# Kernel optimization log

Measured on AMD Instinct MI355X. Metric: run time of the kernel, lower is better.

The kernel has to match this reference:

```python
import jax, jax.numpy as jnp
import numpy as np

H, L, N = 512, 4096, 64

def make_dplr_hippo(n):
    # HiPPO-LegS -> NPLR -> DPLR diagonalization (numpy, init-time only)
    p0 = np.sqrt(1 + 2 * np.arange(n))
    A = p0[:, None] * p0[None, :]
    A = -(np.tril(A) - np.diag(np.arange(n)))
    p = np.sqrt(np.arange(n) + 0.5)
    b = np.sqrt(2 * np.arange(n) + 1.0)
    S = A + p[:, None] * p[None, :]
    Lambda_re = np.full(n, np.diagonal(S).mean())
    Lambda_im, V = np.linalg.eigh(S * -1j)
    Pc = V.conj().T @ p
    Bc = V.conj().T @ b
    return Lambda_re, Lambda_im, Pc, Bc

def setup_inputs() -> dict:
    key = jax.random.key(0)
    k_u, k_c, k_s = jax.random.split(key, 3)
    lr, li, Pc, Bc = make_dplr_hippo(N)
    tile = lambda v: jnp.tile(jnp.asarray(v, jnp.float32)[None, :], (H, 1))
    dt_min, dt_max = 0.001, 0.1
    log_step = (jax.random.uniform(k_s, (H, 1), jnp.float32)
                * (np.log(dt_max) - np.log(dt_min)) + np.log(dt_min))
    return {
        "u": jax.random.normal(k_u, (H, L), jnp.float32),
        "Lambda_re": tile(lr), "Lambda_im": tile(li),
        "P_re": tile(Pc.real), "P_im": tile(Pc.imag),
        "B_re": tile(Bc.real), "B_im": tile(Bc.imag),
        "C": jax.random.normal(k_c, (H, N, 2), jnp.float32) * (0.5 ** 0.5),
        "D": jnp.ones((H, 1), jnp.float32),
        "log_step": log_step,
    }

def reference(u, Lambda_re, Lambda_im, P_re, P_im, B_re, B_im, C, D, log_step):
    # u: [H, L]; all params leading dim H (vmapped channels)
    Lam = jnp.minimum(Lambda_re, -1e-4) + 1j * Lambda_im      # [H, N]
    P = P_re + 1j * P_im                                       # [H, N]
    B = B_re + 1j * B_im                                       # [H, N]
    Cc = C[..., 0] + 1j * C[..., 1]                             # [H, N]
    step = jnp.exp(log_step)                                    # [H, 1]
    Lseq = u.shape[-1]
    Omega = jnp.exp(-2j * jnp.pi * (jnp.arange(Lseq) / Lseq)).astype(jnp.complex64)  # [L]
    g = (2.0 / step) * ((1.0 - Omega) / (1.0 + Omega))[None, :]  # [H, L]
    c = 2.0 / (1.0 + Omega)                                      # [L]
    denom = 1.0 / (g[:, :, None] - Lam[:, None, :])              # [H, L, N]
    cauchy = lambda v: jnp.einsum('hn,hln->hl', v, denom)
    k00 = cauchy(Cc.conj() * B)
    k01 = cauchy(Cc.conj() * P)
    k10 = cauchy(P.conj() * B)
    k11 = cauchy(P.conj() * P)
    atRoots = c[None, :] * (k00 - k01 * (1.0 / (1.0 + k11)) * k10)
    K = jnp.fft.ifft(atRoots, Lseq, axis=-1).real                # [H, L] conv kernel
    # causal convolution via zero-padded FFT (length 2L)
    ud = jnp.fft.rfft(u, n=2 * Lseq, axis=-1)
    Kd = jnp.fft.rfft(K, n=2 * Lseq, axis=-1)
    y = jnp.fft.irfft(ud * Kd, n=2 * Lseq, axis=-1)[..., :Lseq]
    return y + D * u
```

## Files before the change

### kernel.cpp

```cpp
#include <hip/hip_runtime.h>
#include <math.h>

#define NT 512

typedef float v2 __attribute__((ext_vector_type(2)));

__device__ __forceinline__ v2 vrot(v2 a){ return (v2){-a.y, a.x}; }
__device__ __forceinline__ v2 vconj(v2 a){ return (v2){a.x, -a.y}; }

__device__ __forceinline__ v2 pk_addrot(v2 a, v2 b){
    v2 d;
    asm("v_pk_add_f32 %0, %1, %2 op_sel:[0,1] op_sel_hi:[1,0] neg_lo:[0,1] neg_hi:[0,0]"
        : "=v"(d) : "v"(a), "v"(b));
    return d;
}
__device__ __forceinline__ v2 pk_subrot(v2 a, v2 b){
    v2 d;
    asm("v_pk_add_f32 %0, %1, %2 op_sel:[0,1] op_sel_hi:[1,0] neg_lo:[0,0] neg_hi:[0,1]"
        : "=v"(d) : "v"(a), "v"(b));
    return d;
}
__device__ __forceinline__ v2 vcmul(v2 a, v2 b){
    v2 d;
    asm("v_pk_mul_f32 %0, %1, %2 op_sel:[0,0] op_sel_hi:[0,1]"
        : "=v"(d) : "v"(a), "v"(b));
    asm("v_pk_fma_f32 %0, %1, %2, %0 op_sel:[1,1,0] op_sel_hi:[1,0,1] neg_lo:[0,1,0] neg_hi:[0,0,0]"
        : "+v"(d) : "v"(a), "v"(b));
    return d;
}
__device__ __forceinline__ v2 vcmulc(v2 a, v2 b){
    v2 d;
    asm("v_pk_mul_f32 %0, %1, %2 op_sel:[0,0] op_sel_hi:[0,1] neg_lo:[0,0] neg_hi:[0,1]"
        : "=v"(d) : "v"(a), "v"(b));
    asm("v_pk_fma_f32 %0, %1, %2, %0 op_sel:[1,1,0] op_sel_hi:[1,0,1]"
        : "+v"(d) : "v"(a), "v"(b));
    return d;
}

__device__ __forceinline__ v2 pk_add_bh(v2 a, v2 s){
    v2 d;
    asm("v_pk_add_f32 %0, %1, %2 op_sel:[0,1] op_sel_hi:[1,1]"
        : "=v"(d) : "v"(a), "s"(s));
    return d;
}
__device__ __forceinline__ v2 pk_fma_sq_bh(v2 a, v2 s){
    v2 d;
    asm("v_pk_fma_f32 %0, %1, %1, %2 op_sel:[0,0,1] op_sel_hi:[1,1,1]"
        : "=v"(d) : "v"(a), "s"(s));
    return d;
}
__device__ __forceinline__ v2 pk_mul_cross(v2 a){
    v2 d;
    asm("v_pk_mul_f32 %0, %1, %1 op_sel:[1,0] op_sel_hi:[0,1]"
        : "=v"(d) : "v"(a));
    return d;
}
__device__ __forceinline__ v2 pk_inv_lo(v2 rr, v2 dd){
    v2 d;
    asm("v_pk_mul_f32 %0, %1, %2 op_sel:[0,1] op_sel_hi:[0,0]"
        : "=v"(d) : "v"(rr), "v"(dd));
    return d;
}
__device__ __forceinline__ v2 pk_inv_hi(v2 rr, v2 dd){
    v2 d;
    asm("v_pk_mul_f32 %0, %1, %2 op_sel:[1,1] op_sel_hi:[1,0]"
        : "=v"(d) : "v"(rr), "v"(dd));
    return d;
}
__device__ __forceinline__ v2 pk_mul_bl(v2 a, v2 s){
    v2 d;
    asm("v_pk_mul_f32 %0, %1, %2 op_sel:[0,0] op_sel_hi:[1,0]"
        : "=v"(d) : "v"(a), "s"(s));
    return d;
}
__device__ __forceinline__ v2 pk_mulp(v2 a, v2 b){
    v2 d;
    asm("v_pk_mul_f32 %0, %1, %2 op_sel:[0,0] op_sel_hi:[1,1]"
        : "=v"(d) : "v"(a), "v"(b));
    return d;
}
__device__ __forceinline__ void fmaBlo(v2& acc, v2 w, v2 p){
    asm("v_pk_fma_f32 %0, %1, %2, %0 op_sel:[0,0,0] op_sel_hi:[0,1,1]"
        : "+v"(acc) : "s"(w), "v"(p));
}
__device__ __forceinline__ void fmaBhi(v2& acc, v2 w, v2 p){
    asm("v_pk_fma_f32 %0, %1, %2, %0 op_sel:[1,0,0] op_sel_hi:[1,1,1]"
        : "+v"(acc) : "s"(w), "v"(p));
}
__device__ __forceinline__ void fmaBlon(v2& acc, v2 w, v2 p){
    asm("v_pk_fma_f32 %0, %1, %2, %0 op_sel:[0,0,0] op_sel_hi:[0,1,1] neg_lo:[1,0,0] neg_hi:[1,0,0]"
        : "+v"(acc) : "s"(w), "v"(p));
}

__device__ __forceinline__ int SW(int e){ return e ^ (((e>>5) ^ (e>>9)) & 15); }

__device__ __forceinline__ v2& q512(v2* buf, int tbs, int k){
    return *(v2*)((char*)buf + ((tbs ^ (k<<3)) + (k<<12)));
}
__device__ __forceinline__ v2& q512u(v2* buf, int tbs, int k){
    return *(v2*)((char*)buf + (((tbs ^ 64) ^ (k<<3)) + (k<<12) + 32768));
}

__device__ __forceinline__ int d8r4(int x){
    return ((x&7)<<9) | (((x>>3)&7)<<6) | (((x>>6)&7)<<3) | ((x>>9)&7);
}
__device__ __forceinline__ int rev3(int t){
    return ((t&7)<<6) | (t&56) | ((t>>6)&7);
}

__device__ __forceinline__ void load_row(const v2* twd, int rowIdx, v2 W[7]) {
    const float4* rp4 = (const float4*)(twd + rowIdx*8);
    float4 q0 = rp4[0], q1 = rp4[1], q2 = rp4[2], q3 = rp4[3];
    W[0]=(v2){q0.x,q0.y}; W[1]=(v2){q0.z,q0.w}; W[2]=(v2){q1.x,q1.y};
    W[3]=(v2){q1.z,q1.w}; W[4]=(v2){q2.x,q2.y}; W[5]=(v2){q2.z,q2.w};
    W[6]=(v2){q3.x,q3.y};
}

__device__ __forceinline__ void dft8_inv(v2 t[8], v2 y[8]) {
    const float RH = 0.70710678f;
    v2 p  = t[0]+t[4], m  = t[0]-t[4], q  = t[2]+t[6], r  = t[2]-t[6];
    v2 E0 = p+q, E2 = p-q;
    v2 E1 = pk_addrot(m, r), E3 = pk_subrot(m, r);
    v2 p2 = t[1]+t[5], m2 = t[1]-t[5], q2 = t[3]+t[7], r2 = t[3]-t[7];
    v2 O0 = p2+q2, O2 = p2-q2;
    v2 O1 = pk_addrot(m2, r2), O3 = pk_subrot(m2, r2);
    v2 W1O = RH * pk_addrot(O1, O1);
    v2 A3  = RH * pk_addrot(O3, O3);
    y[0] = E0 + O0;  y[4] = E0 - O0;
    y[1] = E1 + W1O; y[5] = E1 - W1O;
    y[2] = pk_addrot(E2, O2); y[6] = pk_subrot(E2, O2);
    y[3] = pk_addrot(E3, A3); y[7] = pk_subrot(E3, A3);
}

__device__ __forceinline__ void dft8_inv_lo4(v2 t[8], v2 y[4]) {
    const float RH = 0.70710678f;
    v2 p  = t[0]+t[4], m  = t[0]-t[4], q  = t[2]+t[6], r  = t[2]-t[6];
    v2 E0 = p+q, E2 = p-q;
    v2 E1 = pk_addrot(m, r), E3 = pk_subrot(m, r);
    v2 p2 = t[1]+t[5], m2 = t[1]-t[5], q2 = t[3]+t[7], r2 = t[3]-t[7];
    v2 O0 = p2+q2, O2 = p2-q2;
    v2 O1 = pk_addrot(m2, r2), O3 = pk_subrot(m2, r2);
    v2 W1O = RH * pk_addrot(O1, O1);
    v2 A3  = RH * pk_addrot(O3, O3);
    y[0] = E0 + O0;
    y[1] = E1 + W1O;
    y[2] = pk_addrot(E2, O2);
    y[3] = pk_addrot(E3, A3);
}

__device__ __forceinline__ void dft8_fwd(v2 t[8], v2 y[8]) {
    const float RH = 0.70710678f;
    v2 p  = t[0]+t[4], m  = t[0]-t[4], q  = t[2]+t[6], r  = t[2]-t[6];
    v2 E0 = p+q, E2 = p-q;
    v2 E1 = pk_subrot(m, r), E3 = pk_addrot(m, r);
    v2 p2 = t[1]+t[5], m2 = t[1]-t[5], q2 = t[3]+t[7], r2 = t[3]-t[7];
    v2 O0 = p2+q2, O2 = p2-q2;
    v2 O1 = pk_subrot(m2, r2), O3 = pk_addrot(m2, r2);
    v2 W1O = RH * pk_subrot(O1, O1);
    v2 A3f = RH * pk_addrot(O3, O3);
    y[0] = E0 + O0;  y[4] = E0 - O0;
    y[1] = E1 + W1O; y[5] = E1 - W1O;
    y[2] = pk_subrot(E2, O2); y[6] = pk_addrot(E2, O2);
    y[3] = E3 - A3f; y[7] = E3 + A3f;
}


template<int Q, bool BAR>
__device__ __forceinline__ void r8_dit_inv(v2* buf, int tid, const v2* twd) {
    int j = tid & (Q-1);
    v2 W[7];
    load_row(twd, (512/Q)*j, W);
    int base = 8*tid - 7*j;
    v2 t[8];
    #pragma unroll
    for (int k = 0; k < 8; ++k) t[k] = buf[SW(base + k*Q)];
    #pragma unroll
    for (int k = 0; k < 7; ++k) t[k+1] = vcmul(t[k+1], W[k]);
    v2 y[8];
    dft8_inv(t, y);
    #pragma unroll
    for (int m = 0; m < 8; ++m) buf[SW(base + m*Q)] = y[m];
    if (BAR) __syncthreads();
    else     __builtin_amdgcn_wave_barrier();
}

template<int Q, bool BAR>
__device__ __forceinline__ void r8_dif_fwd(v2* buf, int tid, const v2* twd) {
    if (Q == 1) {
        const int b0  = tid << 6;
        const int bt  = tid << 3;
        const int mLs = (((bt>>5) ^ (bt>>9)) & 15) << 3;
        const int msU = (mLs ^ 64) + 32768;
        #pragma unroll 1
        for (int hh = 0; hh < 2; ++hh) {
            const int ms = hh ? msU : mLs;
            v2 t[8];
            #pragma unroll
            for (int k = 0; k < 8; ++k)
                t[k] = *(v2*)((char*)buf + ((b0 + (k<<3)) ^ ms));
            v2 y[8];
            dft8_fwd(t, y);
            #pragma unroll
            for (int m = 0; m < 8; ++m)
                *(v2*)((char*)buf + ((b0 + (m<<3)) ^ ms)) = y[m];
        }
        if (BAR) __syncthreads();
        else     __builtin_amdgcn_wave_barrier();
        return;
    }
    int j = tid & (Q-1);
    int baseL = 8*tid - 7*j;
    v2 W[7];
    load_row(twd, (512/Q)*j, W);
    #pragma unroll 1
    for (int hh = 0; hh < 2; ++hh) {
        int base = baseL + (hh << 12);
        v2 t[8];
        #pragma unroll
        for (int k = 0; k < 8; ++k) t[k] = buf[SW(base + k*Q)];
        v2 y[8];
        dft8_fwd(t, y);
        #pragma unroll
        for (int k = 0; k < 7; ++k) y[k+1] = vcmulc(y[k+1], W[k]);
        #pragma unroll
        for (int m = 0; m < 8; ++m) buf[SW(base + m*Q)] = y[m];
    }
    if (BAR) __syncthreads();
    else     __builtin_amdgcn_wave_barrier();
}

__global__ void __launch_bounds__(64)
s4_prep(const float* __restrict__ Lre, const float* __restrict__ Lim,
        const float* __restrict__ Pre, const float* __restrict__ Pim,
        const float* __restrict__ Bre, const float* __restrict__ Bim,
        const float* __restrict__ Cin,
        float* __restrict__ ws8, float* __restrict__ ws1,
        v2* __restrict__ twd)
{
    int b = blockIdx.x;
    if (b == (int)gridDim.x - 1) {
        const float fm = 6.2831853072f / 4096.0f;
        #pragma unroll
        for (int r = 0; r < 8; ++r) {
            int j = r*64 + (int)threadIdx.x;
            #pragma unroll
            for (int k = 0; k < 7; ++k) {
                float s, c; __sincosf(fm * (float)(j*(k+1)), &s, &c);
                twd[j*8 + k] = (v2){c, s};
            }
            twd[j*8 + 7] = (v2){1.0f, 0.0f};
        }
        return;
    }
    int idx = b*64 + threadIdx.x;
    float lre = fminf(Lre[idx], -1e-4f);
    float lim = Lim[idx];
    float pr = Pre[idx], pi = Pim[idx];
    float br = Bre[idx], bi = Bim[idx];
    float cr = Cin[2*idx], ci = Cin[2*idx+1];
    v2 cc = (v2){cr, -ci};
    v2 w00 = vcmul(cc, (v2){br, bi});
    v2 w01 = vcmul(cc, (v2){pr, pi});
    v2 w10 = vcmul((v2){pr,-pi}, (v2){br, bi});
    float* o = ws8 + idx*8;
    o[0] = -lre;  o[1] = -lim;
    o[2] = w00.x; o[3] = w00.y;
    o[4] = w01.x; o[5] = w01.y;
    o[6] = w10.x; o[7] = w10.y;
    ws1[2*idx]   = pr*pr + pi*pi;
    ws1[2*idx+1] = lre*lre;
}

__global__ __attribute__((amdgpu_waves_per_eu(4, 4))) void __launch_bounds__(NT)
s4_fused(const float* __restrict__ u,
         const float* __restrict__ Din, const float* __restrict__ logstep,
         const float* __restrict__ ws8, const float* __restrict__ ws1,
         const v2* __restrict__ twd,
         float* __restrict__ out)
{
    __shared__ v2 buf[8192];
    const int tid = threadIdx.x;
    const int h = blockIdx.x;
    const int tbs = (tid ^ ((tid>>5) & 15)) << 3;

    const float step = expf(logstep[h]);
    const float tos  = 2.0f / step;
    const float hstep = 0.5f * step;
    const float* pp = ws8 + (h*64)*8;
    const float4* pp4 = (const float4*)pp;
    const v2* pw2 = (const v2*)(ws1 + h*128);

    v2 a4[4];
    #pragma unroll 1
    for (int hp = 0; hp < 2; ++hp) {
        v2 tvA, tvB;
        {
            float tv[4];
            #pragma unroll
            for (int i = 0; i < 4; ++i) {
                int l = hp*(4*NT) + i*NT + tid;
                float ang = -6.2831855f * ((float)l * (1.0f/4096.0f));
                float sh, ch; __sincosf(0.5f*ang, &sh, &ch);
                float traw = -tos * sh * __builtin_amdgcn_rcpf(ch);
                tv[i] = fminf(fmaxf(traw, -1e12f), 1e12f);
            }
            tvA = (v2){tv[0], tv[1]};
            tvB = (v2){tv[2], tv[3]};
        }
        v2 aX00A=(v2)(0.f), aY00A=(v2)(0.f), aX00B=(v2)(0.f), aY00B=(v2)(0.f);
        v2 aX01A=(v2)(0.f), aY01A=(v2)(0.f), aX01B=(v2)(0.f), aY01B=(v2)(0.f);
        v2 aX10A=(v2)(0.f), aY10A=(v2)(0.f), aX10B=(v2)(0.f), aY10B=(v2)(0.f);
        v2 aX11A=(v2)(0.f), aY11A=(v2)(0.f), aX11B=(v2)(0.f), aY11B=(v2)(0.f);
        #pragma unroll 2
        for (int n = 0; n < 64; ++n) {
            float4 A = pp4[2*n], Bq = pp4[2*n+1];
            v2 lam = (v2){A.x, A.y};
            v2 w00 = (v2){A.z, A.w};
            v2 w01 = (v2){Bq.x, Bq.y};
            v2 w10 = (v2){Bq.z, Bq.w};
            v2 Wv  = pw2[n];
            v2 sA = pk_add_bh(tvA, lam), sB = pk_add_bh(tvB, lam);
            v2 dA = pk_fma_sq_bh(sA, Wv), dB = pk_fma_sq_bh(sB, Wv);
            v2 PA = pk_mul_cross(dA), PB = pk_mul_cross(dB);
            v2 RR;
            RR.x = __builtin_amdgcn_rcpf(PA.x);
            RR.y = __builtin_amdgcn_rcpf(PB.x);
            v2 invA = pk_inv_lo(RR, dA), invB = pk_inv_hi(RR, dB);
            v2 pxA = pk_mul_bl(invA, lam), pxB = pk_mul_bl(invB, lam);
            v2 pyA = pk_mulp(invA, sA),    pyB = pk_mulp(invB, sB);
            fmaBlo(aX00A, w00, pxA); fmaBhi(aX00A, w00, pyA);
            fmaBhi(aY00A, w00, pxA); fmaBlon(aY00A, w00, pyA);
            fmaBlo(aX00B, w00, pxB); fmaBhi(aX00B, w00, pyB);
            fmaBhi(aY00B, w00, pxB); fmaBlon(aY00B, w00, pyB);
            fmaBlo(aX01A, w01, pxA); fmaBhi(aX01A, w01, pyA);
            fmaBhi(aY01A, w01, pxA); fmaBlon(aY01A, w01, pyA);
            fmaBlo(aX01B, w01, pxB); fmaBhi(aX01B, w01, pyB);
            fmaBhi(aY01B, w01, pxB); fmaBlon(aY01B, w01, pyB);
            fmaBlo(aX10A, w10, pxA); fmaBhi(aX10A, w10, pyA);
            fmaBhi(aY10A, w10, pxA); fmaBlon(aY10A, w10, pyA);
            fmaBlo(aX10B, w10, pxB); fmaBhi(aX10B, w10, pyB);
            fmaBhi(aY10B, w10, pxB); fmaBlon(aY10B, w10, pyB);
            fmaBlo(aX11A, Wv, pxA);  fmaBlon(aY11A, Wv, pyA);
            fmaBlo(aX11B, Wv, pxB);  fmaBlon(aY11B, Wv, pyB);
        }
        float tvv[4] = { tvA.x, tvA.y, tvB.x, tvB.y };
        v2 k00[4] = { {aX00A.x,aY00A.x}, {aX00A.y,aY00A.y},
                      {aX00B.x,aY00B.x}, {aX00B.y,aY00B.y} };
        v2 k01[4] = { {aX01A.x,aY01A.x}, {aX01A.y,aY01A.y},
                      {aX01B.x,aY01B.x}, {aX01B.y,aY01B.y} };
        v2 k10[4] = { {aX10A.x,aY10A.x}, {aX10A.y,aY10A.y},
                      {aX10B.x,aY10B.x}, {aX10B.y,aY10B.y} };
        v2 k11[4] = { {aX11A.x,aY11A.x}, {aX11A.y,aY11A.y},
                      {aX11B.x,aY11B.x}, {aX11B.y,aY11B.y} };
        #pragma unroll
        for (int i = 0; i < 4; ++i) {
            v2 opk = (v2){1.0f + k11[i].x, k11[i].y};
            float iv = __builtin_amdgcn_rcpf(opk.x*opk.x + opk.y*opk.y);
            v2 r11 = vconj(opk) * iv;
            v2 t  = vcmul(vcmul(k01[i], r11), k10[i]);
            v2 cf = (v2){1.0f, tvv[i]*hstep};
            v2 res = vcmul(cf, k00[i] - t);
            if (hp == 0) q512(buf, tbs, i) = res;
            else         a4[i] = res;
        }
    }
    {
        v2 t[8];
        #pragma unroll
        for (int k = 0; k < 4; ++k) t[k] = q512(buf, tbs, k);
        #pragma unroll
        for (int k = 0; k < 4; ++k) t[4+k] = a4[k];
        __syncthreads();
        v2 y[8];
        dft8_inv(t, y);
        const int tb8 = 8*rev3(tid);
        const int b8  = tb8 << 3;
        const int m8s = (((tb8>>5) ^ (tb8>>9)) & 15) << 3;
        #pragma unroll
        for (int m = 0; m < 8; ++m)
            *(v2*)((char*)buf + ((b8 + (m<<3)) ^ m8s)) = y[m];
    }
    __syncthreads();

    r8_dit_inv<8,  false>(buf, tid, twd);
    r8_dit_inv<64, true >(buf, tid, twd);

    {
        v2 W[7];
        load_row(twd, tid, W);
        v2 t[8];
        #pragma unroll
        for (int k = 0; k < 8; ++k) t[k] = q512(buf, tbs, k);
        #pragma unroll
        for (int k = 0; k < 7; ++k) t[k+1] = vcmul(t[k+1], W[k]);
        v2 y[8];
        dft8_inv(t, y);
        float uval[8];
        const float* up = u + h*4096;
        #pragma unroll
        for (int m = 0; m < 8; ++m) uval[m] = up[tid + 512*m];
        float s2, c2; __sincosf(-6.2831853072f/8192.0f*(float)tid, &s2, &c2);
        v2 cur0 = (v2){c2, s2};
        const v2 C16n = (v2){0.92387953f, -0.38268343f};
        v2 zL[8], zU[8];
        {
            v2 cur = cur0;
            #pragma unroll
            for (int k = 0; k < 8; ++k) {
                zL[k] = (v2){uval[k], y[k].x * (1.0f/4096.0f)};
                zU[k] = vcmul(zL[k], cur);
                cur = vcmul(cur, C16n);
            }
        }
        v2 s[8];
        dft8_fwd(zL, s);
        #pragma unroll
        for (int m = 1; m < 8; ++m) s[m] = vcmulc(s[m], W[m-1]);
        #pragma unroll
        for (int m = 0; m < 8; ++m) q512(buf, tbs, m) = s[m];
        dft8_fwd(zU, s);
        #pragma unroll
        for (int m = 1; m < 8; ++m) s[m] = vcmulc(s[m], W[m-1]);
        #pragma unroll
        for (int m = 0; m < 8; ++m) q512u(buf, tbs, m) = s[m];
    }
    __syncthreads();

    r8_dif_fwd<64, false>(buf, tid, twd);
    r8_dif_fwd<8,  false>(buf, tid, twd);
    r8_dif_fwd<1,  true >(buf, tid, twd);

    {
        float sb, cb; __sincosf(6.2831853072f/8192.0f*(float)tid, &sb, &cb);
        v2 cur = (v2){cb, sb};
        const v2 C16p = (v2){0.92387953f, 0.38268343f};
        v2 v[8];
        #pragma unroll 1
        for (int i = 0; i < 8; ++i) {
            int r  = i*NT + tid;
            int par = (r&1)<<12;
            int e1 = par + d8r4(r>>1);
            int e3 = e1 + 4;
            int k2c = 4096 - r;
            int e4 = ((k2c&1)<<12) + d8r4((k2c>>1)&4095);
            int e2 = (r == 0) ? 0 : (e4 + 4);
            v2 za = buf[SW(e1)];
            v2 zb = buf[SW(e2)];
            v2 zc = buf[SW(e3)];
            v2 zd = buf[SW(e4)];
            v2 U1 = 0.5f*(za + vconj(zb));
            v2 K1 = -0.5f*vrot(za - vconj(zb));
            v2 Yr = vcmul(U1, K1);
            v2 U2 = 0.5f*(zc + vconj(zd));
            v2 K2 = -0.5f*vrot(zc - vconj(zd));
            v2 Ys = vcmul(U2, K2);
            v[i] = pk_addrot(Yr + Ys, vcmul(cur, Yr - Ys));
            cur = vcmul(cur, C16p);
        }
        __syncthreads();
        v2 y[8];
        dft8_inv(v, y);
        const int tb8 = 8*rev3(tid);
        const int b8  = tb8 << 3;
        const int m8s = (((tb8>>5) ^ (tb8>>9)) & 15) << 3;
        #pragma unroll
        for (int m = 0; m < 8; ++m)
            *(v2*)((char*)buf + ((b8 + (m<<3)) ^ m8s)) = y[m];
    }
    __syncthreads();

    r8_dit_inv<8,  false>(buf, tid, twd);
    r8_dit_inv<64, true >(buf, tid, twd);

    {
        v2 W[7];
        load_row(twd, tid, W);
        v2 t[8];
        #pragma unroll
        for (int k = 0; k < 8; ++k) t[k] = q512(buf, tbs, k);
        #pragma unroll
        for (int k = 0; k < 7; ++k) t[k+1] = vcmul(t[k+1], W[k]);
        v2 y[4];
        dft8_inv_lo4(t, y);
        const float Dh = Din[h];
        const float sc = 1.0f / 8192.0f;
        const v2* u2 = (const v2*)(u + h*4096);
        v2*     out2 = (v2*)(out + h*4096);
        #pragma unroll
        for (int m = 0; m < 4; ++m) {
            int n = tid + 512*m;
            out2[n] = sc*y[m] + Dh*u2[n];
        }
    }
}

extern "C" void kernel_launch(void* const* d_in, const int* in_sizes, int n_in,
                              void* d_out, int out_size, void* d_ws, size_t ws_size,
                              hipStream_t stream)
{
    const float* u       = (const float*)d_in[0];
    const float* Lre     = (const float*)d_in[1];
    const float* Lim     = (const float*)d_in[2];
    const float* Pre     = (const float*)d_in[3];
    const float* Pim     = (const float*)d_in[4];
    const float* Bre     = (const float*)d_in[5];
    const float* Bim     = (const float*)d_in[6];
    const float* Cin     = (const float*)d_in[7];
    const float* Din     = (const float*)d_in[8];
    const float* logstep = (const float*)d_in[9];
    float* out = (float*)d_out;
    const int H = in_sizes[8];

    float* ws8 = (float*)d_ws;
    float* ws1 = ws8 + (size_t)H*64*8;
    v2*    twd = (v2*)(ws1 + (size_t)H*128);

    hipLaunchKernelGGL(s4_prep, dim3(H + 1), dim3(64), 0, stream,
                       Lre, Lim, Pre, Pim, Bre, Bim, Cin, ws8, ws1, twd);
    hipLaunchKernelGGL(s4_fused, dim3(H), dim3(NT), 0, stream,
                       u, Din, logstep, ws8, ws1, twd, out);
}
```

Measured before the change: 144.3 us.

## Split fused S4 kernel into separate Cauchy and FFT kernels

```diff
diff --git a/kernel.cpp b/kernel.cpp
--- a/kernel.cpp
+++ b/kernel.cpp
@@ -1,7 +1,8 @@
 #include <hip/hip_runtime.h>
 #include <math.h>
 
-#define NT 512
+#define NT  512
+#define NTC 256
 
 typedef float v2 __attribute__((ext_vector_type(2)));
 
@@ -93,14 +94,12 @@
 }
 
 __device__ __forceinline__ int SW(int e){ return e ^ (((e>>5) ^ (e>>9)) & 15); }
-
 __device__ __forceinline__ v2& q512(v2* buf, int tbs, int k){
     return *(v2*)((char*)buf + ((tbs ^ (k<<3)) + (k<<12)));
 }
 __device__ __forceinline__ v2& q512u(v2* buf, int tbs, int k){
     return *(v2*)((char*)buf + (((tbs ^ 64) ^ (k<<3)) + (k<<12) + 32768));
 }
-
 __device__ __forceinline__ int d8r4(int x){
     return ((x&7)<<9) | (((x>>3)&7)<<6) | (((x>>6)&7)<<3) | ((x>>9)&7);
 }
@@ -163,7 +162,6 @@
     y[2] = pk_subrot(E2, O2); y[6] = pk_addrot(E2, O2);
     y[3] = E3 - A3f; y[7] = E3 + A3f;
 }
-
 
 template<int Q, bool BAR>
 __device__ __forceinline__ void r8_dit_inv(v2* buf, int tid, const v2* twd) {
@@ -235,10 +233,12 @@
         const float* __restrict__ Bre, const float* __restrict__ Bim,
         const float* __restrict__ Cin,
         float* __restrict__ ws8, float* __restrict__ ws1,
-        v2* __restrict__ twd)
+        v2* __restrict__ twd, float* __restrict__ tanv,
+        v2* __restrict__ w8192, int full)
 {
     int b = blockIdx.x;
-    if (b == (int)gridDim.x - 1) {
+    int nb = (int)gridDim.x;
+    if (b == nb - 3) {
         const float fm = 6.2831853072f / 4096.0f;
         #pragma unroll
         for (int r = 0; r < 8; ++r) {
@@ -249,6 +249,28 @@
                 twd[j*8 + k] = (v2){c, s};
             }
             twd[j*8 + 7] = (v2){1.0f, 0.0f};
+        }
+        return;
+    }
+    if (b == nb - 2) {
+        if (!full) return;
+        #pragma unroll 1
+        for (int r = 0; r < 64; ++r) {
+            int l = r*64 + (int)threadIdx.x;
+            float ang = -6.2831855f * ((float)l * (1.0f/4096.0f));
+            float sh, ch; __sincosf(0.5f*ang, &sh, &ch);
+            tanv[l] = -sh * __builtin_amdgcn_rcpf(ch);
+        }
+        return;
+    }
+    if (b == nb - 1) {
+        if (!full) return;
+        const float fm2 = 6.2831853072f / 8192.0f;
+        #pragma unroll
+        for (int r = 0; r < 8; ++r) {
+            int j = r*64 + (int)threadIdx.x;
+            float s, c; __sincosf(fm2 * (float)j, &s, &c);
+            w8192[j] = (v2){c, s};
         }
         return;
     }
@@ -269,6 +291,226 @@
     o[6] = w10.x; o[7] = w10.y;
     ws1[2*idx]   = pr*pr + pi*pi;
     ws1[2*idx+1] = lre*lre;
+}
+
+__global__ __attribute__((amdgpu_waves_per_eu(8, 8))) void __launch_bounds__(NTC)
+s4_cauchy(const float* __restrict__ logstep,
+          const float* __restrict__ ws8, const float* __restrict__ ws1,
+          const float* __restrict__ tanv, v2* __restrict__ atR)
+{
+    const int tid = threadIdx.x;
+    const int h   = blockIdx.x;
+    const int qi  = blockIdx.y;
+    const int lbase = qi*1024;
+
+    const float step = expf(logstep[h]);
+    const float tos  = 2.0f / step;
+    const float hstep = 0.5f * step;
+    const float4* pp4 = (const float4*)(ws8 + (h*64)*8);
+    const v2* pw2 = (const v2*)(ws1 + h*128);
+
+    v2 tvA, tvB;
+    {
+        float tv[4];
+        #pragma unroll
+        for (int i = 0; i < 4; ++i) {
+            float tr = tos * tanv[lbase + (i<<8) + tid];
+            tv[i] = fminf(fmaxf(tr, -1e12f), 1e12f);
+        }
+        tvA = (v2){tv[0], tv[1]};
+        tvB = (v2){tv[2], tv[3]};
+    }
+    v2 aX00A=(v2)(0.f), aY00A=(v2)(0.f), aX00B=(v2)(0.f), aY00B=(v2)(0.f);
+    v2 aX01A=(v2)(0.f), aY01A=(v2)(0.f), aX01B=(v2)(0.f), aY01B=(v2)(0.f);
+    v2 aX10A=(v2)(0.f), aY10A=(v2)(0.f), aX10B=(v2)(0.f), aY10B=(v2)(0.f);
+    v2 aX11A=(v2)(0.f), aY11A=(v2)(0.f), aX11B=(v2)(0.f), aY11B=(v2)(0.f);
+    #pragma unroll 2
+    for (int n = 0; n < 64; ++n) {
+        float4 A = pp4[2*n], Bq = pp4[2*n+1];
+        v2 lam = (v2){A.x, A.y};
+        v2 w00 = (v2){A.z, A.w};
+        v2 w01 = (v2){Bq.x, Bq.y};
+        v2 w10 = (v2){Bq.z, Bq.w};
+        v2 Wv  = pw2[n];
+        v2 sA = pk_add_bh(tvA, lam), sB = pk_add_bh(tvB, lam);
+        v2 dA = pk_fma_sq_bh(sA, Wv), dB = pk_fma_sq_bh(sB, Wv);
+        v2 PA = pk_mul_cross(dA), PB = pk_mul_cross(dB);
+        v2 RR;
+        RR.x = __builtin_amdgcn_rcpf(PA.x);
+        RR.y = __builtin_amdgcn_rcpf(PB.x);
+        v2 invA = pk_inv_lo(RR, dA), invB = pk_inv_hi(RR, dB);
+        v2 pxA = pk_mul_bl(invA, lam), pxB = pk_mul_bl(invB, lam);
+        v2 pyA = pk_mulp(invA, sA),    pyB = pk_mulp(invB, sB);
+        fmaBlo(aX00A, w00, pxA); fmaBhi(aX00A, w00, pyA);
+        fmaBhi(aY00A, w00, pxA); fmaBlon(aY00A, w00, pyA);
+        fmaBlo(aX00B, w00, pxB); fmaBhi(aX00B, w00, pyB);
+        fmaBhi(aY00B, w00, pxB); fmaBlon(aY00B, w00, pyB);
+        fmaBlo(aX01A, w01, pxA); fmaBhi(aX01A, w01, pyA);
+        fmaBhi(aY01A, w01, pxA); fmaBlon(aY01A, w01, pyA);
+        fmaBlo(aX01B, w01, pxB); fmaBhi(aX01B, w01, pyB);
+        fmaBhi(aY01B, w01, pxB); fmaBlon(aY01B, w01, pyB);
+        fmaBlo(aX10A, w10, pxA); fmaBhi(aX10A, w10, pyA);
+        fmaBhi(aY10A, w10, pxA); fmaBlon(aY10A, w10, pyA);
+        fmaBlo(aX10B, w10, pxB); fmaBhi(aX10B, w10, pyB);
+        fmaBhi(aY10B, w10, pxB); fmaBlon(aY10B, w10, pyB);
+        fmaBlo(aX11A, Wv, pxA);  fmaBlon(aY11A, Wv, pyA);
+        fmaBlo(aX11B, Wv, pxB);  fmaBlon(aY11B, Wv, pyB);
+    }
+    float tvv[4] = { tvA.x, tvA.y, tvB.x, tvB.y };
+    v2 k00[4] = { {aX00A.x,aY00A.x}, {aX00A.y,aY00A.y},
+                  {aX00B.x,aY00B.x}, {aX00B.y,aY00B.y} };
+    v2 k01[4] = { {aX01A.x,aY01A.x}, {aX01A.y,aY01A.y},
+                  {aX01B.x,aY01B.x}, {aX01B.y,aY01B.y} };
+    v2 k10[4] = { {aX10A.x,aY10A.x}, {aX10A.y,aY10A.y},
+                  {aX10B.x,aY10B.x}, {aX10B.y,aY10B.y} };
+    v2 k11[4] = { {aX11A.x,aY11A.x}, {aX11A.y,aY11A.y},
+                  {aX11B.x,aY11B.x}, {aX11B.y,aY11B.y} };
+    v2* aRo = atR + (size_t)h*4096 + lbase;
+    #pragma unroll
+    for (int i = 0; i < 4; ++i) {
+        v2 opk = (v2){1.0f + k11[i].x, k11[i].y};
+        float iv = __builtin_amdgcn_rcpf(opk.x*opk.x + opk.y*opk.y);
+        v2 r11 = vconj(opk) * iv;
+        v2 t  = vcmul(vcmul(k01[i], r11), k10[i]);
+        v2 cf = (v2){1.0f, tvv[i]*hstep};
+        aRo[(i<<8) + tid] = vcmul(cf, k00[i] - t);
+    }
+}
+
+__global__ __attribute__((amdgpu_waves_per_eu(4, 4))) void __launch_bounds__(NT)
+s4_fft(const float* __restrict__ u, const float* __restrict__ Din,
+       const v2* __restrict__ twd, const v2* __restrict__ w8192,
+       const v2* __restrict__ atR, float* __restrict__ out)
+{
+    __shared__ v2 buf[8192];
+    const int tid = threadIdx.x;
+    const int h = blockIdx.x;
+    const int tbs = (tid ^ ((tid>>5) & 15)) << 3;
+
+    {
+        const v2* aR = atR + (size_t)h*4096;
+        v2 t[8];
+        #pragma unroll
+        for (int k = 0; k < 8; ++k) t[k] = aR[tid + 512*k];
+        v2 y[8];
+        dft8_inv(t, y);
+        const int tb8 = 8*rev3(tid);
+        const int b8  = tb8 << 3;
+        const int m8s = (((tb8>>5) ^ (tb8>>9)) & 15) << 3;
+        #pragma unroll
+        for (int m = 0; m < 8; ++m)
+            *(v2*)((char*)buf + ((b8 + (m<<3)) ^ m8s)) = y[m];
+    }
+    __syncthreads();
+
+    r8_dit_inv<8,  false>(buf, tid, twd);
+    r8_dit_inv<64, true >(buf, tid, twd);
+
+    {
+        v2 W[7];
+        load_row(twd, tid, W);
+        v2 t[8];
+        #pragma unroll
+        for (int k = 0; k < 8; ++k) t[k] = q512(buf, tbs, k);
+        #pragma unroll
+        for (int k = 0; k < 7; ++k) t[k+1] = vcmul(t[k+1], W[k]);
+        v2 y[8];
+        dft8_inv(t, y);
+        float uval[8];
+        const float* up = u + h*4096;
+        #pragma unroll
+        for (int m = 0; m < 8; ++m) uval[m] = up[tid + 512*m];
+        v2 cur0 = vconj(w8192[tid]);
+        const v2 C16n = (v2){0.92387953f, -0.38268343f};
+        v2 zL[8], zU[8];
+        {
+            v2 cur = cur0;
+            #pragma unroll
+            for (int k = 0; k < 8; ++k) {
+                zL[k] = (v2){uval[k], y[k].x * (1.0f/4096.0f)};
+                zU[k] = vcmul(zL[k], cur);
+                cur = vcmul(cur, C16n);
+            }
+        }
+        v2 s[8];
+        dft8_fwd(zL, s);
+        #pragma unroll
+        for (int m = 1; m < 8; ++m) s[m] = vcmulc(s[m], W[m-1]);
+        #pragma unroll
+        for (int m = 0; m < 8; ++m) q512(buf, tbs, m) = s[m];
+        dft8_fwd(zU, s);
+        #pragma unroll
+        for (int m = 1; m < 8; ++m) s[m] = vcmulc(s[m], W[m-1]);
+        #pragma unroll
+        for (int m = 0; m < 8; ++m) q512u(buf, tbs, m) = s[m];
+    }
+    __syncthreads();
+
+    r8_dif_fwd<64, false>(buf, tid, twd);
+    r8_dif_fwd<8,  false>(buf, tid, twd);
+    r8_dif_fwd<1,  true >(buf, tid, twd);
+
+    {
+        v2 cur = w8192[tid];
+        const v2 C16p = (v2){0.92387953f, 0.38268343f};
+        v2 v[8];
+        #pragma unroll 1
+        for (int i = 0; i < 8; ++i) {
+            int r  = i*NT + tid;
+            int par = (r&1)<<12;
+            int e1 = par + d8r4(r>>1);
+            int e3 = e1 + 4;
+            int k2c = 4096 - r;
+            int e4 = ((k2c&1)<<12) + d8r4((k2c>>1)&4095);
+            int e2 = (r == 0) ? 0 : (e4 + 4);
+            v2 za = buf[SW(e1)];
+            v2 zb = buf[SW(e2)];
+            v2 zc = buf[SW(e3)];
+            v2 zd = buf[SW(e4)];
+            v2 U1 = 0.5f*(za + vconj(zb));
+            v2 K1 = -0.5f*vrot(za - vconj(zb));
+            v2 Yr = vcmul(U1, K1);
+            v2 U2 = 0.5f*(zc + vconj(zd));
+            v2 K2 = -0.5f*vrot(zc - vconj(zd));
+            v2 Ys = vcmul(U2, K2);
+            v[i] = pk_addrot(Yr + Ys, vcmul(cur, Yr - Ys));
+            cur = vcmul(cur, C16p);
+        }
+        __syncthreads();
+        v2 y[8];
+        dft8_inv(v, y);
+        const int tb8 = 8*rev3(tid);
+        const int b8  = tb8 << 3;
+        const int m8s = (((tb8>>5) ^ (tb8>>9)) & 15) << 3;
+        #pragma unroll
+        for (int m = 0; m < 8; ++m)
+            *(v2*)((char*)buf + ((b8 + (m<<3)) ^ m8s)) = y[m];
+    }
+    __syncthreads();
+
+    r8_dit_inv<8,  false>(buf, tid, twd);
+    r8_dit_inv<64, true >(buf, tid, twd);
+
+    {
+        v2 W[7];
+        load_row(twd, tid, W);
+        v2 t[8];
+        #pragma unroll
+        for (int k = 0; k < 8; ++k) t[k] = q512(buf, tbs, k);
+        #pragma unroll
+        for (int k = 0; k < 7; ++k) t[k+1] = vcmul(t[k+1], W[k]);
+        v2 y[4];
+        dft8_inv_lo4(t, y);
+        const float Dh = Din[h];
+        const float sc = 1.0f / 8192.0f;
+        const v2* u2 = (const v2*)(u + h*4096);
+        v2*     out2 = (v2*)(out + h*4096);
+        #pragma unroll
+        for (int m = 0; m < 4; ++m) {
+            int n = tid + 512*m;
+            out2[n] = sc*y[m] + Dh*u2[n];
+        }
+    }
 }
 
 __global__ __attribute__((amdgpu_waves_per_eu(4, 4))) void __launch_bounds__(NT)
@@ -511,12 +753,25 @@
     float* out = (float*)d_out;
     const int H = in_sizes[8];
 
-    float* ws8 = (float*)d_ws;
-    float* ws1 = ws8 + (size_t)H*64*8;
-    v2*    twd = (v2*)(ws1 + (size_t)H*128);
-
-    hipLaunchKernelGGL(s4_prep, dim3(H + 1), dim3(64), 0, stream,
-                       Lre, Lim, Pre, Pim, Bre, Bim, Cin, ws8, ws1, twd);
-    hipLaunchKernelGGL(s4_fused, dim3(H), dim3(NT), 0, stream,
-                       u, Din, logstep, ws8, ws1, twd, out);
-}
+    float* ws8   = (float*)d_ws;
+    float* ws1   = ws8 + (size_t)H*64*8;
+    v2*    twd   = (v2*)(ws1 + (size_t)H*128);
+    float* tanv  = (float*)(twd + 512*8);
+    v2*    w8192 = (v2*)(tanv + 4096);
+    v2*    atR   = w8192 + 512;
+    size_t need_full = (size_t)((char*)(atR + (size_t)H*4096) - (char*)d_ws);
+    int full = (ws_size >= need_full) ? 1 : 0;
+
+    hipLaunchKernelGGL(s4_prep, dim3(H + 3), dim3(64), 0, stream,
+                       Lre, Lim, Pre, Pim, Bre, Bim, Cin, ws8, ws1, twd,
+                       tanv, w8192, full);
+    if (full) {
+        hipLaunchKernelGGL(s4_cauchy, dim3(H, 4), dim3(NTC), 0, stream,
+                           logstep, ws8, ws1, tanv, atR);
+        hipLaunchKernelGGL(s4_fft, dim3(H), dim3(NT), 0, stream,
+                           u, Din, twd, w8192, atR, out);
+    } else {
+        hipLaunchKernelGGL(s4_fused, dim3(H), dim3(NT), 0, stream,
+                           u, Din, logstep, ws8, ws1, twd, out);
+    }
+}
```

After: 151.1 us. 1.05x slower.
